# Kernel optimization log

Hardware: AMD Instinct MI355X
Metric: run time of the kernel (lower is better)

## Reference

```python
import jax, jax.numpy as jnp
import numpy as np


def conv1d(x, w, b, pad):
    # x: [B, Cin, T], w: [Cout, Cin, K]
    y = jax.lax.conv_general_dilated(x, w, window_strides=(1,), padding=[(pad, pad)],
                                     dimension_numbers=('NCH', 'OIH', 'NCH'))
    return y + b[None, :, None]


def setup_inputs() -> dict:
    key = jax.random.key(0)
    ks = jax.random.split(key, 16)
    B, T1, T2 = 32, 2048, 512
    Cmel, Ctext, Catt = 100, 512, 100
    s = 0.05
    inp = {
        'queries': jax.random.normal(ks[0], (B, Cmel, T1), dtype=jnp.float32),
        'keys': jax.random.normal(ks[1], (B, Ctext, T2), dtype=jnp.float32),
        'query_lens': jax.random.randint(ks[2], (B,), 1, T1),
        'mask': jax.random.randint(ks[3], (B, T2, 1), 0, 2).astype(bool),
        'attn_prior': jax.random.uniform(ks[4], (B, T1, T2), dtype=jnp.float32),
        # key_proj: ConvNorm(512->1024, k=3) -> ReLU -> ConvNorm(1024->100, k=1)
        'kW1': jax.random.normal(ks[5], (Ctext * 2, Ctext, 3), dtype=jnp.float32) * s,
        'kb1': jnp.zeros((Ctext * 2,), dtype=jnp.float32),
        'kW2': jax.random.normal(ks[6], (Catt, Ctext * 2, 1), dtype=jnp.float32) * s,
        'kb2': jnp.zeros((Catt,), dtype=jnp.float32),
        # query_proj: ConvNorm(100->200, k=3) -> ReLU -> ConvNorm(200->100, k=1) -> ReLU -> ConvNorm(100->100, k=1)
        'qW1': jax.random.normal(ks[7], (Cmel * 2, Cmel, 3), dtype=jnp.float32) * s,
        'qb1': jnp.zeros((Cmel * 2,), dtype=jnp.float32),
        'qW2': jax.random.normal(ks[8], (Cmel, Cmel * 2, 1), dtype=jnp.float32) * s,
        'qb2': jnp.zeros((Cmel,), dtype=jnp.float32),
        'qW3': jax.random.normal(ks[9], (Catt, Cmel, 1), dtype=jnp.float32) * s,
        'qb3': jnp.zeros((Catt,), dtype=jnp.float32),
    }
    return inp


def reference(queries, keys, query_lens, mask, attn_prior,
              kW1, kb1, kW2, kb2, qW1, qb1, qW2, qb2, qW3, qb3):
    # key projection -> [B, Catt, T2]
    k = jax.nn.relu(conv1d(keys, kW1, kb1, 1))
    k = conv1d(k, kW2, kb2, 0)
    # query projection -> [B, Catt, T1]
    q = jax.nn.relu(conv1d(queries, qW1, qb1, 1))
    q = jax.nn.relu(conv1d(q, qW2, qb2, 0))
    q = conv1d(q, qW3, qb3, 0)
    q2 = jnp.sum(q * q, axis=1)                      # [B, T1]
    k2 = jnp.sum(k * k, axis=1)                      # [B, T2]
    qk = jnp.einsum('bct,bcs->bts', q, k)            # [B, T1, T2]
    attn = -0.0005 * (q2[:, :, None] + k2[:, None, :] - 2.0 * qk)[:, None]  # [B,1,T1,T2]
    attn = jax.nn.log_softmax(attn, axis=3) + jnp.log(attn_prior[:, None] + 1e-8)
    attn_logprob = attn
    m = jnp.transpose(mask, (0, 2, 1))[:, :, None, :]  # [B,1,1,T2], True = masked
    attn = jnp.where(m, -jnp.inf, attn)
    attn = jax.nn.softmax(attn, axis=3)
    return attn, attn_logprob
```

## Files before the change

kernel.cpp:

```cpp
#include <hip/hip_runtime.h>
#include <cstdint>

#define B_   32
#define T1_  2048
#define T2_  512

typedef __attribute__((ext_vector_type(8))) short short8;
typedef __attribute__((ext_vector_type(4))) float f32x4;

__device__ __forceinline__ unsigned short f2bf(float f) {
    union { float f; unsigned u; } x; x.f = f;
    unsigned r = x.u + 0x7fffu + ((x.u >> 16) & 1u);
    return (unsigned short)(r >> 16);
}
__device__ __forceinline__ float bf2f(unsigned short u) {
    union { unsigned u; float f; } x; x.u = ((unsigned)u) << 16;
    return x.f;
}

__device__ __forceinline__ void async16(const unsigned short* g, unsigned short* l) {
    __builtin_amdgcn_global_load_lds(
        (const __attribute__((address_space(1))) unsigned int*)g,
        (__attribute__((address_space(3))) unsigned int*)l, 16, 0, 0);
}

__global__ __launch_bounds__(256) void prep_kernel(
    const float* __restrict__ queries, const float* __restrict__ keys,
    const float* __restrict__ kW1, const float* __restrict__ kW2,
    const float* __restrict__ qW1, const float* __restrict__ qW2,
    const float* __restrict__ qW3,
    unsigned short* __restrict__ keysT, unsigned short* __restrict__ queriesT,
    unsigned short* __restrict__ Wdst)
{
    __shared__ float tile[32][33];
    const int blk = blockIdx.x, tid = threadIdx.x;
    if (blk < 4096) {
        const float* X; unsigned short* Y; int C, Cp, T, ntx, ty, tx0, b;
        if (blk < 2048) {
            X = keys; Y = keysT; C = 512; Cp = 512; T = 512; ntx = 16;
            b = blk >> 6; int rem = blk & 63; ty = rem >> 2; tx0 = (rem & 3) * 4;
        } else {
            int f = blk - 2048;
            X = queries; Y = queriesT; C = 100; Cp = 128; T = 2048; ntx = 64;
            b = f >> 6; int rem = f & 63; ty = rem & 3; tx0 = (rem >> 2) * 4;
        }
        const int c0 = ty * 32;
        const int cl = tid >> 5, tl = tid & 31;
        for (int tx = tx0; tx < tx0 + 4; ++tx) {
            const int t0 = tx * 32;
            __syncthreads();
#pragma unroll
            for (int i = 0; i < 4; ++i) {
                int c = c0 + cl + i * 8;
                float v = (c < C) ? X[((size_t)b * C + c) * T + t0 + tl] : 0.f;
                tile[cl + i * 8][tl] = v;
            }
            __syncthreads();
#pragma unroll
            for (int i = 0; i < 4; ++i) {
                int tw = cl + i * 8, cw = tl;
                Y[((size_t)b * (T + 2) + t0 + tw + 1) * Cp + c0 + cw] = f2bf(tile[cw][tw]);
            }
            if (tid < 32) {
                if (tx == 0)       Y[((size_t)b * (T + 2)) * Cp + c0 + tid] = 0;
                if (tx == ntx - 1) Y[((size_t)b * (T + 2) + T + 1) * Cp + c0 + tid] = 0;
            }
        }
    } else {
        size_t base = (size_t)(blk - 4096) * 2048 + (size_t)tid * 8;
#pragma unroll
        for (int j = 0; j < 8; ++j) {
            size_t idx = base + j;
            float v = 0.f;
            if (idx < 1572864) {
                int dk = (int)(idx / 524288); int rem = (int)(idx % 524288);
                int m = rem >> 9, ci = rem & 511;
                v = kW1[((size_t)m * 512 + ci) * 3 + dk];
            } else if (idx < 1703936) {
                int r = (int)(idx - 1572864); int m = r >> 10, c = r & 1023;
                if (m < 100) v = kW2[(size_t)m * 1024 + c];
            } else if (idx < 1802240) {
                int r = (int)(idx - 1703936); int dk = r / 32768, rem = r % 32768;
                int m = rem >> 7, ci = rem & 127;
                if (m < 200 && ci < 100) v = qW1[((size_t)m * 100 + ci) * 3 + dk];
            } else if (idx < 1835008) {
                int r = (int)(idx - 1802240); int m = r >> 8, c = r & 255;
                if (m < 100 && c < 200) v = qW2[(size_t)m * 200 + c];
            } else if (idx < 1851392) {
                int r = (int)(idx - 1835008); int m = r >> 7, c = r & 127;
                if (m < 100 && c < 100) v = qW3[(size_t)m * 100 + c];
            } else {
                continue;
            }
            Wdst[idx] = f2bf(v);
        }
    }
}

struct GArgs {
    const unsigned short* A;
    const unsigned short* Bm;
    const float* bias;
    unsigned short* Y;
    float* nrm;
    int Ck, N, Mpad, nx, relu, norm, Cout;
};

template<int KW>
__global__ __launch_bounds__(256) void gemm_pair(GArgs g0, GArgs g1, int n0)
{
    __shared__ __align__(16) unsigned char smem[36352];
    unsigned short* Al = (unsigned short*)smem;
    unsigned short* Bl = Al + 8192;
    unsigned short* Ct = (unsigned short*)smem;
    float* biasS = (float*)(smem + 34816);
    float* normS = (float*)(smem + 35328);

    const bool first = (blockIdx.x < (unsigned)n0);
    const GArgs g = first ? g0 : g1;
    const int idx = first ? blockIdx.x : (blockIdx.x - n0);
    const int ny = g.Mpad >> 7;
    const int per_b = g.nx * ny;
    const int b = idx / per_b; const int rem = idx - b * per_b;
    const int y = rem / g.nx, x = rem - y * g.nx;
    const int co0 = y * 128, t0 = x * 128;

    const int tid = threadIdx.x;
    const int wave = tid >> 6, lane = tid & 63;
    const int lm = lane & 15, kg = lane >> 4;
    const int mbase = (wave >> 1) * 64, nbase = (wave & 1) * 64;

    if (tid < 128) biasS[tid] = (co0 + tid < g.Cout) ? g.bias[co0 + tid] : 0.f;

    const int r7 = lane >> 3;
    const int s7 = lane & 7;
    const int swz = ((s7 ^ r7) * 8);
    const int Ck = g.Ck;

    f32x4 acc[4][4];
#pragma unroll
    for (int mi = 0; mi < 4; ++mi)
#pragma unroll
        for (int ni = 0; ni < 4; ++ni) acc[mi][ni] = (f32x4){0.f, 0.f, 0.f, 0.f};

#pragma unroll 1
    for (int dk = 0; dk < KW; ++dk) {
        const unsigned short* Ad = g.A + ((size_t)dk * g.Mpad + co0) * Ck;
        const unsigned short* Bd = g.Bm +
            ((size_t)b * (g.N + (KW == 3 ? 2 : 0)) + t0 + dk) * Ck;
        for (int kk = 0; kk < Ck; kk += 64) {
            __syncthreads();
#pragma unroll
            for (int i = 0; i < 4; ++i) {
                int R0 = wave * 32 + i * 8;
                async16(Ad + (size_t)(R0 + r7) * Ck + kk + swz, Al + R0 * 64);
                async16(Bd + (size_t)(R0 + r7) * Ck + kk + swz, Bl + R0 * 64);
            }
            __syncthreads();
#pragma unroll
            for (int kk2 = 0; kk2 < 2; ++kk2) {
                short8 av[4], bv[4];
#pragma unroll
                for (int mi = 0; mi < 4; ++mi) {
                    int row = mbase + mi * 16 + lm;
                    av[mi] = *(const short8*)(Al + row * 64 +
                                              (((kk2 * 4 + kg) ^ (lm & 7)) * 8));
                }
#pragma unroll
                for (int ni = 0; ni < 4; ++ni) {
                    int row = nbase + ni * 16 + lm;
                    bv[ni] = *(const short8*)(Bl + row * 64 +
                                              (((kk2 * 4 + kg) ^ (lm & 7)) * 8));
                }
#pragma unroll
                for (int mi = 0; mi < 4; ++mi)
#pragma unroll
                    for (int ni = 0; ni < 4; ++ni)
                        acc[mi][ni] = __builtin_amdgcn_mfma_f32_16x16x32_bf16(
                            av[mi], bv[ni], acc[mi][ni], 0, 0, 0);
            }
        }
    }
    __syncthreads();

    float sq[4] = {0.f, 0.f, 0.f, 0.f};
#pragma unroll
    for (int mi = 0; mi < 4; ++mi)
#pragma unroll
        for (int ni = 0; ni < 4; ++ni)
#pragma unroll
            for (int r = 0; r < 4; ++r) {
                int co_l = mbase + mi * 16 + kg * 4 + r;
                int t_l  = nbase + ni * 16 + lm;
                float v = acc[mi][ni][r] + biasS[co_l];
                if (g.relu) v = fmaxf(v, 0.f);
                Ct[t_l * 136 + co_l] = f2bf(v);
                sq[ni] += v * v;
            }
    if (g.norm) {
#pragma unroll
        for (int ni = 0; ni < 4; ++ni) {
            float s = sq[ni];
            s += __shfl_xor(s, 16, 64);
            s += __shfl_xor(s, 32, 64);
            if (kg == 0) normS[(wave >> 1) * 128 + nbase + ni * 16 + lm] = s;
        }
    }
    __syncthreads();
    unsigned short* Yb = g.Y + ((size_t)b * g.N + t0) * g.Mpad + co0;
    int c0 = (tid & 15) * 8;
#pragma unroll
    for (int p = 0; p < 8; ++p) {
        int r = (tid >> 4) + p * 16;
        *(uint4*)(Yb + (size_t)r * g.Mpad + c0) = *(const uint4*)(Ct + r * 136 + c0);
    }
    if (g.norm && tid < 128)
        g.nrm[(size_t)b * g.N + t0 + tid] = normS[tid] + normS[128 + tid];
}

__global__ __launch_bounds__(256) void attn_mfma(
    const unsigned short* __restrict__ q,
    const unsigned short* __restrict__ k,
    const float* __restrict__ q2,
    const float* __restrict__ k2,
    const unsigned char* __restrict__ mask,
    const float* __restrict__ prior,
    float* __restrict__ out_attn, float* __restrict__ out_logp)
{
    __shared__ float redM[4][32], redS[4][32];
    __shared__ float rowA[32], rowB[32];

    const int b = blockIdx.y, t0 = blockIdx.x * 32;
    const int tid = threadIdx.x, wave = tid >> 6, lane = tid & 63;
    const int lm = lane & 15, quad = lane >> 4;
    const float NEG_INF = -__builtin_huge_valf();

    const unsigned short* qb = q + ((size_t)b * T1_ + t0) * 128;
    short8 af[2][4];
#pragma unroll
    for (int mi = 0; mi < 2; ++mi)
#pragma unroll
        for (int kb = 0; kb < 4; ++kb)
            af[mi][kb] = *(const short8*)(qb + (size_t)(mi * 16 + lm) * 128 + kb * 32 + quad * 8);

    f32x4 acc[2][8];
#pragma unroll
    for (int mi = 0; mi < 2; ++mi)
#pragma unroll
        for (int nf = 0; nf < 8; ++nf) acc[mi][nf] = (f32x4){0.f, 0.f, 0.f, 0.f};

    const unsigned short* kp = k + ((size_t)b * T2_ + wave * 128) * 128;
#pragma unroll
    for (int nf = 0; nf < 8; ++nf) {
        short8 bfr[4];
#pragma unroll
        for (int kb = 0; kb < 4; ++kb)
            bfr[kb] = *(const short8*)(kp + (size_t)(nf * 16 + lm) * 128 + kb * 32 + quad * 8);
#pragma unroll
        for (int mi = 0; mi < 2; ++mi)
#pragma unroll
            for (int kb = 0; kb < 4; ++kb)
                acc[mi][nf] = __builtin_amdgcn_mfma_f32_16x16x32_bf16(
                    af[mi][kb], bfr[kb], acc[mi][nf], 0, 0, 0);
    }

    float k2v[8];
    unsigned char mk[8];
#pragma unroll
    for (int nf = 0; nf < 8; ++nf) {
        int col = wave * 128 + nf * 16 + lm;
        k2v[nf] = k2[b * T2_ + col];
        mk[nf]  = mask[b * T2_ + col];
    }
    float q2v[2][4];
#pragma unroll
    for (int mi = 0; mi < 2; ++mi)
#pragma unroll
        for (int r = 0; r < 4; ++r)
            q2v[mi][r] = q2[b * T1_ + t0 + mi * 16 + quad * 4 + r];
#pragma unroll
    for (int mi = 0; mi < 2; ++mi)
#pragma unroll
        for (int nf = 0; nf < 8; ++nf)
#pragma unroll
            for (int r = 0; r < 4; ++r)
                acc[mi][nf][r] = 1e-3f * acc[mi][nf][r] - 5e-4f * (q2v[mi][r] + k2v[nf]);

#pragma unroll
    for (int mi = 0; mi < 2; ++mi)
#pragma unroll
        for (int r = 0; r < 4; ++r) {
            float m = NEG_INF;
#pragma unroll
            for (int nf = 0; nf < 8; ++nf) m = fmaxf(m, acc[mi][nf][r]);
#pragma unroll
            for (int d = 1; d <= 8; d <<= 1) m = fmaxf(m, __shfl_xor(m, d, 64));
            float s = 0.f;
#pragma unroll
            for (int nf = 0; nf < 8; ++nf) s += __expf(acc[mi][nf][r] - m);
#pragma unroll
            for (int d = 1; d <= 8; d <<= 1) s += __shfl_xor(s, d, 64);
            if (lm == 0) {
                redM[wave][mi * 16 + quad * 4 + r] = m;
                redS[wave][mi * 16 + quad * 4 + r] = s;
            }
        }
    __syncthreads();
    if (tid < 32) {
        float m = redM[0][tid];
        m = fmaxf(m, redM[1][tid]); m = fmaxf(m, redM[2][tid]); m = fmaxf(m, redM[3][tid]);
        float s = 0.f;
#pragma unroll
        for (int w = 0; w < 4; ++w) s += redS[w][tid] * __expf(redM[w][tid] - m);
        rowA[tid] = m + __logf(s);
    }
    __syncthreads();
    float L1[2][4];
#pragma unroll
    for (int mi = 0; mi < 2; ++mi)
#pragma unroll
        for (int r = 0; r < 4; ++r) L1[mi][r] = rowA[mi * 16 + quad * 4 + r];

    const size_t base = ((size_t)b * T1_ + t0) * T2_;
#pragma unroll
    for (int mi = 0; mi < 2; ++mi)
#pragma unroll
        for (int r = 0; r < 4; ++r) {
            size_t rowoff = base + (size_t)(mi * 16 + quad * 4 + r) * T2_;
#pragma unroll
            for (int nf = 0; nf < 8; ++nf) {
                int col = wave * 128 + nf * 16 + lm;
                float pv = prior[rowoff + col];
                float t = acc[mi][nf][r] + __logf(pv + 1e-8f);
                out_logp[rowoff + col] = t - L1[mi][r];
                acc[mi][nf][r] = mk[nf] ? NEG_INF : t;
            }
        }

#pragma unroll
    for (int mi = 0; mi < 2; ++mi)
#pragma unroll
        for (int r = 0; r < 4; ++r) {
            float m = NEG_INF;
#pragma unroll
            for (int nf = 0; nf < 8; ++nf) m = fmaxf(m, acc[mi][nf][r]);
#pragma unroll
            for (int d = 1; d <= 8; d <<= 1) m = fmaxf(m, __shfl_xor(m, d, 64));
            float s = 0.f;
#pragma unroll
            for (int nf = 0; nf < 8; ++nf) s += __expf(acc[mi][nf][r] - m);
#pragma unroll
            for (int d = 1; d <= 8; d <<= 1) s += __shfl_xor(s, d, 64);
            if (lm == 0) {
                redM[wave][mi * 16 + quad * 4 + r] = m;
                redS[wave][mi * 16 + quad * 4 + r] = s;
            }
        }
    __syncthreads();
    if (tid < 32) {
        float m = redM[0][tid];
        m = fmaxf(m, redM[1][tid]); m = fmaxf(m, redM[2][tid]); m = fmaxf(m, redM[3][tid]);
        float s = 0.f;
#pragma unroll
        for (int w = 0; w < 4; ++w) s += redS[w][tid] * __expf(redM[w][tid] - m);
        rowA[tid] = m;
        rowB[tid] = 1.0f / s;
    }
    __syncthreads();

#pragma unroll
    for (int mi = 0; mi < 2; ++mi)
#pragma unroll
        for (int r = 0; r < 4; ++r) {
            int rl = mi * 16 + quad * 4 + r;
            float m2 = rowA[rl], is2 = rowB[rl];
            size_t rowoff = base + (size_t)rl * T2_;
#pragma unroll
            for (int nf = 0; nf < 8; ++nf) {
                int col = wave * 128 + nf * 16 + lm;
                out_attn[rowoff + col] = __expf(acc[mi][nf][r] - m2) * is2;
            }
        }
}

extern "C" void kernel_launch(void* const* d_in, const int* in_sizes, int n_in,
                              void* d_out, int out_size, void* d_ws, size_t ws_size,
                              hipStream_t stream)
{
    const float* queries = (const float*)d_in[0];
    const float* keys    = (const float*)d_in[1];
    const unsigned char* mask = (const unsigned char*)d_in[3];
    const float* prior   = (const float*)d_in[4];
    const float* kW1 = (const float*)d_in[5];
    const float* kb1 = (const float*)d_in[6];
    const float* kW2 = (const float*)d_in[7];
    const float* kb2 = (const float*)d_in[8];
    const float* qW1 = (const float*)d_in[9];
    const float* qb1 = (const float*)d_in[10];
    const float* qW2 = (const float*)d_in[11];
    const float* qb2 = (const float*)d_in[12];
    const float* qW3 = (const float*)d_in[13];
    const float* qb3 = (const float*)d_in[14];

    unsigned short* ws = (unsigned short*)d_ws;
    unsigned short* keysT    = ws;
    unsigned short* queriesT = ws + 8421376;
    unsigned short* Bmat2    = ws + 16818176;
    unsigned short* Bmat4    = ws + 33595392;
    unsigned short* Bmat5    = ws + 50372608;
    unsigned short* q_att    = ws + 58761216;
    unsigned short* k_att    = ws + 67149824;
    unsigned short* Wdst     = ws + 69246976;
    unsigned short* Wk1s = Wdst;
    unsigned short* Wk2  = Wdst + 1572864;
    unsigned short* Wq1s = Wdst + 1703936;
    unsigned short* Wq2  = Wdst + 1802240;
    unsigned short* Wq3  = Wdst + 1835008;
    float* q2f = (float*)(ws + 71098368);
    float* k2f = q2f + 65536;

    float* out_attn = (float*)d_out;
    float* out_logp = (float*)d_out + (size_t)B_ * T1_ * T2_;

    dim3 blk(256);
    prep_kernel<<<dim3(5120), blk, 0, stream>>>(queries, keys, kW1, kW2, qW1, qW2, qW3,
                                                keysT, queriesT, Wdst);

    GArgs a_key1 = {Wk1s, keysT,    kb1, Bmat2, nullptr, 512,  512, 1024,  4, 1, 0, 1024};
    GArgs a_q1   = {Wq1s, queriesT, qb1, Bmat4, nullptr, 128, 2048,  256, 16, 1, 0,  200};
    gemm_pair<3><<<dim3(2048), blk, 0, stream>>>(a_key1, a_q1, 1024);

    GArgs a_key2 = {Wk2, Bmat2, kb2, k_att, k2f,     1024,  512, 128,  4, 0, 1, 100};
    GArgs a_q2   = {Wq2, Bmat4, qb2, Bmat5, nullptr,  256, 2048, 128, 16, 1, 0, 100};
    gemm_pair<1><<<dim3(640), blk, 0, stream>>>(a_key2, a_q2, 128);

    GArgs a_q3   = {Wq3, Bmat5, qb3, q_att, q2f, 128, 2048, 128, 16, 0, 1, 100};
    gemm_pair<1><<<dim3(512), blk, 0, stream>>>(a_q3, a_q3, 512);

    attn_mfma<<<dim3(T1_ / 32, B_), blk, 0, stream>>>(q_att, k_att, q2f, k2f, mask, prior,
                                                      out_attn, out_logp);

    (void)in_sizes; (void)n_in; (void)out_size; (void)ws_size;
}
```

Before: 597.0 us.

## Double-buffer GEMM LDS loads and fuse query conv2+conv3 in one kernel

Splits the GEMM k-loop into a double-buffered LDS pipeline, so the async global-to-LDS load for the next step is issued while MFMAs run on the current buffer. This roughly halves the barriers per step. It also fuses the second and third query 1x1 convolutions: the ReLU'd output tile stays in LDS and is multiplied by Wq3 inside the same block. That removes one kernel launch and the round-trip of the intermediate buffer through global memory. LDS use grows from about 36 KB to 67 KB per block, which may lower occupancy.

Result: no change. 591.3 us (-0.9%).

```diff
diff --git a/kernel.cpp b/kernel.cpp
--- a/kernel.cpp
+++ b/kernel.cpp
@@ -12,10 +12,6 @@
     union { float f; unsigned u; } x; x.f = f;
     unsigned r = x.u + 0x7fffu + ((x.u >> 16) & 1u);
     return (unsigned short)(r >> 16);
-}
-__device__ __forceinline__ float bf2f(unsigned short u) {
-    union { unsigned u; float f; } x; x.u = ((unsigned)u) << 16;
-    return x.f;
 }
 
 __device__ __forceinline__ void async16(const unsigned short* g, unsigned short* l) {
@@ -104,17 +100,22 @@
     unsigned short* Y;
     float* nrm;
     int Ck, N, Mpad, nx, relu, norm, Cout;
+    const unsigned short* A2;
+    const float* bias2;
+    unsigned short* Y2;
+    float* nrm2;
+    int fuse;
 };
 
 template<int KW>
 __global__ __launch_bounds__(256) void gemm_pair(GArgs g0, GArgs g1, int n0)
 {
-    __shared__ __align__(16) unsigned char smem[36352];
+    __shared__ __align__(16) unsigned char smem[67584];
     unsigned short* Al = (unsigned short*)smem;
-    unsigned short* Bl = Al + 8192;
     unsigned short* Ct = (unsigned short*)smem;
-    float* biasS = (float*)(smem + 34816);
-    float* normS = (float*)(smem + 35328);
+    float* biasS  = (float*)(smem + 65536);
+    float* bias2S = (float*)(smem + 66048);
+    float* normS  = (float*)(smem + 66560);
 
     const bool first = (blockIdx.x < (unsigned)n0);
     const GArgs g = first ? g0 : g1;
@@ -130,12 +131,34 @@
     const int lm = lane & 15, kg = lane >> 4;
     const int mbase = (wave >> 1) * 64, nbase = (wave & 1) * 64;
 
-    if (tid < 128) biasS[tid] = (co0 + tid < g.Cout) ? g.bias[co0 + tid] : 0.f;
+    if (tid < 128) {
+        biasS[tid] = (co0 + tid < g.Cout) ? g.bias[co0 + tid] : 0.f;
+        if (g.fuse) bias2S[tid] = (tid < 100) ? g.bias2[tid] : 0.f;
+    }
 
     const int r7 = lane >> 3;
     const int s7 = lane & 7;
     const int swz = ((s7 ^ r7) * 8);
     const int Ck = g.Ck;
+    const int ksteps = Ck >> 6;
+    const int kshift = __builtin_ctz(ksteps);
+    const int nsteps = KW * ksteps;
+
+    auto stage = [&](int s) {
+        const int dk = s >> kshift;
+        const int kk = (s & (ksteps - 1)) << 6;
+        const unsigned short* Ag = g.A + ((size_t)dk * g.Mpad + co0) * Ck + kk;
+        const unsigned short* Bg = g.Bm +
+            ((size_t)b * (g.N + (KW == 3 ? 2 : 0)) + t0 + dk) * Ck + kk;
+        unsigned short* Ad = Al + (s & 1) * 16384;
+        unsigned short* Bd = Ad + 8192;
+#pragma unroll
+        for (int i = 0; i < 4; ++i) {
+            int R0 = wave * 32 + i * 8;
+            async16(Ag + (size_t)(R0 + r7) * Ck + swz, Ad + R0 * 64);
+            async16(Bg + (size_t)(R0 + r7) * Ck + swz, Bd + R0 * 64);
+        }
+    };
 
     f32x4 acc[4][4];
 #pragma unroll
@@ -143,79 +166,115 @@
 #pragma unroll
         for (int ni = 0; ni < 4; ++ni) acc[mi][ni] = (f32x4){0.f, 0.f, 0.f, 0.f};
 
+    stage(0);
+    __syncthreads();
 #pragma unroll 1
-    for (int dk = 0; dk < KW; ++dk) {
-        const unsigned short* Ad = g.A + ((size_t)dk * g.Mpad + co0) * Ck;
-        const unsigned short* Bd = g.Bm +
-            ((size_t)b * (g.N + (KW == 3 ? 2 : 0)) + t0 + dk) * Ck;
-        for (int kk = 0; kk < Ck; kk += 64) {
-            __syncthreads();
-#pragma unroll
-            for (int i = 0; i < 4; ++i) {
-                int R0 = wave * 32 + i * 8;
-                async16(Ad + (size_t)(R0 + r7) * Ck + kk + swz, Al + R0 * 64);
-                async16(Bd + (size_t)(R0 + r7) * Ck + kk + swz, Bl + R0 * 64);
-            }
-            __syncthreads();
-#pragma unroll
-            for (int kk2 = 0; kk2 < 2; ++kk2) {
-                short8 av[4], bv[4];
-#pragma unroll
-                for (int mi = 0; mi < 4; ++mi) {
-                    int row = mbase + mi * 16 + lm;
-                    av[mi] = *(const short8*)(Al + row * 64 +
-                                              (((kk2 * 4 + kg) ^ (lm & 7)) * 8));
+    for (int s = 0; s < nsteps; ++s) {
+        if (s + 1 < nsteps) stage(s + 1);
+        const unsigned short* Ab = Al + (s & 1) * 16384;
+        const unsigned short* Bb = Ab + 8192;
+#pragma unroll
+        for (int kk2 = 0; kk2 < 2; ++kk2) {
+            short8 av[4], bv[4];
+#pragma unroll
+            for (int mi = 0; mi < 4; ++mi) {
+                int row = mbase + mi * 16 + lm;
+                av[mi] = *(const short8*)(Ab + row * 64 +
+                                          (((kk2 * 4 + kg) ^ (lm & 7)) * 8));
+            }
+#pragma unroll
+            for (int ni = 0; ni < 4; ++ni) {
+                int row = nbase + ni * 16 + lm;
+                bv[ni] = *(const short8*)(Bb + row * 64 +
+                                          (((kk2 * 4 + kg) ^ (lm & 7)) * 8));
+            }
+#pragma unroll
+            for (int mi = 0; mi < 4; ++mi)
+#pragma unroll
+                for (int ni = 0; ni < 4; ++ni)
+                    acc[mi][ni] = __builtin_amdgcn_mfma_f32_16x16x32_bf16(
+                        av[mi], bv[ni], acc[mi][ni], 0, 0, 0);
+        }
+        __syncthreads();
+    }
+
+    auto epi = [&](f32x4 (&A)[4][4], const float* bS, int dorelu, int donorm) {
+        float sq[4] = {0.f, 0.f, 0.f, 0.f};
+#pragma unroll
+        for (int mi = 0; mi < 4; ++mi)
+#pragma unroll
+            for (int ni = 0; ni < 4; ++ni)
+#pragma unroll
+                for (int r = 0; r < 4; ++r) {
+                    int co_l = mbase + mi * 16 + kg * 4 + r;
+                    int t_l  = nbase + ni * 16 + lm;
+                    float v = A[mi][ni][r] + bS[co_l];
+                    if (dorelu) v = fmaxf(v, 0.f);
+                    Ct[t_l * 136 + co_l] = f2bf(v);
+                    sq[ni] += v * v;
                 }
-#pragma unroll
-                for (int ni = 0; ni < 4; ++ni) {
-                    int row = nbase + ni * 16 + lm;
-                    bv[ni] = *(const short8*)(Bl + row * 64 +
-                                              (((kk2 * 4 + kg) ^ (lm & 7)) * 8));
-                }
-#pragma unroll
-                for (int mi = 0; mi < 4; ++mi)
-#pragma unroll
-                    for (int ni = 0; ni < 4; ++ni)
-                        acc[mi][ni] = __builtin_amdgcn_mfma_f32_16x16x32_bf16(
-                            av[mi], bv[ni], acc[mi][ni], 0, 0, 0);
-            }
-        }
-    }
-    __syncthreads();
-
-    float sq[4] = {0.f, 0.f, 0.f, 0.f};
-#pragma unroll
-    for (int mi = 0; mi < 4; ++mi)
-#pragma unroll
-        for (int ni = 0; ni < 4; ++ni)
-#pragma unroll
-            for (int r = 0; r < 4; ++r) {
-                int co_l = mbase + mi * 16 + kg * 4 + r;
-                int t_l  = nbase + ni * 16 + lm;
-                float v = acc[mi][ni][r] + biasS[co_l];
-                if (g.relu) v = fmaxf(v, 0.f);
-                Ct[t_l * 136 + co_l] = f2bf(v);
-                sq[ni] += v * v;
-            }
-    if (g.norm) {
-#pragma unroll
-        for (int ni = 0; ni < 4; ++ni) {
-            float s = sq[ni];
-            s += __shfl_xor(s, 16, 64);
-            s += __shfl_xor(s, 32, 64);
-            if (kg == 0) normS[(wave >> 1) * 128 + nbase + ni * 16 + lm] = s;
-        }
-    }
-    __syncthreads();
-    unsigned short* Yb = g.Y + ((size_t)b * g.N + t0) * g.Mpad + co0;
-    int c0 = (tid & 15) * 8;
-#pragma unroll
-    for (int p = 0; p < 8; ++p) {
-        int r = (tid >> 4) + p * 16;
-        *(uint4*)(Yb + (size_t)r * g.Mpad + c0) = *(const uint4*)(Ct + r * 136 + c0);
-    }
-    if (g.norm && tid < 128)
-        g.nrm[(size_t)b * g.N + t0 + tid] = normS[tid] + normS[128 + tid];
+        if (donorm) {
+#pragma unroll
+            for (int ni = 0; ni < 4; ++ni) {
+                float s = sq[ni];
+                s += __shfl_xor(s, 16, 64);
+                s += __shfl_xor(s, 32, 64);
+                if (kg == 0) normS[(wave >> 1) * 128 + nbase + ni * 16 + lm] = s;
+            }
+        }
+    };
+
+    if (!g.fuse) {
+        epi(acc, biasS, g.relu, g.norm);
+        __syncthreads();
+        unsigned short* Yb = g.Y + ((size_t)b * g.N + t0) * g.Mpad + co0;
+        int c0 = (tid & 15) * 8;
+#pragma unroll
+        for (int p = 0; p < 8; ++p) {
+            int r = (tid >> 4) + p * 16;
+            *(uint4*)(Yb + (size_t)r * g.Mpad + c0) = *(const uint4*)(Ct + r * 136 + c0);
+        }
+        if (g.norm && tid < 128)
+            g.nrm[(size_t)b * g.N + t0 + tid] = normS[tid] + normS[128 + tid];
+    } else {
+        epi(acc, biasS, 1, 0);
+        __syncthreads();
+        f32x4 acc2[4][4];
+#pragma unroll
+        for (int mi = 0; mi < 4; ++mi)
+#pragma unroll
+            for (int ni = 0; ni < 4; ++ni) acc2[mi][ni] = (f32x4){0.f, 0.f, 0.f, 0.f};
+#pragma unroll
+        for (int kk = 0; kk < 128; kk += 32) {
+            short8 av2[4], bv2[4];
+#pragma unroll
+            for (int mi = 0; mi < 4; ++mi)
+                av2[mi] = *(const short8*)(g.A2 +
+                    (size_t)(mbase + mi * 16 + lm) * 128 + kk + kg * 8);
+#pragma unroll
+            for (int ni = 0; ni < 4; ++ni)
+                bv2[ni] = *(const short8*)(Ct +
+                    (nbase + ni * 16 + lm) * 136 + kk + kg * 8);
+#pragma unroll
+            for (int mi = 0; mi < 4; ++mi)
+#pragma unroll
+                for (int ni = 0; ni < 4; ++ni)
+                    acc2[mi][ni] = __builtin_amdgcn_mfma_f32_16x16x32_bf16(
+                        av2[mi], bv2[ni], acc2[mi][ni], 0, 0, 0);
+        }
+        __syncthreads();
+        epi(acc2, bias2S, 0, 1);
+        __syncthreads();
+        unsigned short* Yb = g.Y2 + ((size_t)b * g.N + t0) * 128 + co0;
+        int c0 = (tid & 15) * 8;
+#pragma unroll
+        for (int p = 0; p < 8; ++p) {
+            int r = (tid >> 4) + p * 16;
+            *(uint4*)(Yb + (size_t)r * 128 + c0) = *(const uint4*)(Ct + r * 136 + c0);
+        }
+        if (tid < 128)
+            g.nrm2[(size_t)b * g.N + t0 + tid] = normS[tid] + normS[128 + tid];
+    }
 }
 
 __global__ __launch_bounds__(256) void attn_mfma(
@@ -407,7 +466,6 @@
     unsigned short* queriesT = ws + 8421376;
     unsigned short* Bmat2    = ws + 16818176;
     unsigned short* Bmat4    = ws + 33595392;
-    unsigned short* Bmat5    = ws + 50372608;
     unsigned short* q_att    = ws + 58761216;
     unsigned short* k_att    = ws + 67149824;
     unsigned short* Wdst     = ws + 69246976;
@@ -426,16 +484,17 @@
     prep_kernel<<<dim3(5120), blk, 0, stream>>>(queries, keys, kW1, kW2, qW1, qW2, qW3,
                                                 keysT, queriesT, Wdst);
 
-    GArgs a_key1 = {Wk1s, keysT,    kb1, Bmat2, nullptr, 512,  512, 1024,  4, 1, 0, 1024};
-    GArgs a_q1   = {Wq1s, queriesT, qb1, Bmat4, nullptr, 128, 2048,  256, 16, 1, 0,  200};
+    GArgs a_key1 = {Wk1s, keysT,    kb1, Bmat2, nullptr, 512,  512, 1024,  4, 1, 0, 1024,
+                    nullptr, nullptr, nullptr, nullptr, 0};
+    GArgs a_q1   = {Wq1s, queriesT, qb1, Bmat4, nullptr, 128, 2048,  256, 16, 1, 0,  200,
+                    nullptr, nullptr, nullptr, nullptr, 0};
     gemm_pair<3><<<dim3(2048), blk, 0, stream>>>(a_key1, a_q1, 1024);
 
-    GArgs a_key2 = {Wk2, Bmat2, kb2, k_att, k2f,     1024,  512, 128,  4, 0, 1, 100};
-    GArgs a_q2   = {Wq2, Bmat4, qb2, Bmat5, nullptr,  256, 2048, 128, 16, 1, 0, 100};
-    gemm_pair<1><<<dim3(640), blk, 0, stream>>>(a_key2, a_q2, 128);
-
-    GArgs a_q3   = {Wq3, Bmat5, qb3, q_att, q2f, 128, 2048, 128, 16, 0, 1, 100};
-    gemm_pair<1><<<dim3(512), blk, 0, stream>>>(a_q3, a_q3, 512);
+    GArgs a_key2 = {Wk2, Bmat2, kb2, k_att, k2f,     1024,  512, 128,  4, 0, 1, 100,
+                    nullptr, nullptr, nullptr, nullptr, 0};
+    GArgs a_q23  = {Wq2, Bmat4, qb2, nullptr, nullptr, 256, 2048, 128, 16, 1, 0, 100,
+                    Wq3, qb3, q_att, q2f, 1};
+    gemm_pair<1><<<dim3(640), blk, 0, stream>>>(a_key2, a_q23, 128);
 
     attn_mfma<<<dim3(T1_ / 32, B_), blk, 0, stream>>>(q_att, k_att, q2f, k2f, mask, prior,
                                                       out_attn, out_logp);
```
